# Kernel optimization log

Measured on AMD Instinct MI355X. Metric: run time of the kernel, lower is better.

The kernel has to match this reference:

```python
import jax, jax.numpy as jnp
import numpy as np
import math

B, TQ, TK, D, H, K = 4, 1024, 1536, 1024, 16, 1
DV = D // H * K  # 64
DP = D * K       # projection dim


def setup_inputs() -> dict:
    key = jax.random.key(0)
    ks = jax.random.split(key, 12)
    s = 0.02
    query = jax.random.normal(ks[0], (B, TQ, D), dtype=jnp.float32)
    key_value = jax.random.normal(ks[1], (B, TK, D), dtype=jnp.float32)
    relative = jax.random.normal(ks[2], (B, TK, D), dtype=jnp.float32)
    # Transformer-XL causal mask: query i may attend to key j <= i + mem
    mem = TK - TQ
    i = jnp.arange(TQ)[:, None]
    j = jnp.arange(TK)[None, :]
    mask = jnp.broadcast_to(j > i + mem, (B, TQ, TK))  # True = masked
    Wq = jax.random.normal(ks[3], (D, DP), dtype=jnp.float32) * s
    Wk = jax.random.normal(ks[4], (D, DP), dtype=jnp.float32) * s
    Wv = jax.random.normal(ks[5], (D, DP), dtype=jnp.float32) * s
    Wr = jax.random.normal(ks[6], (D, DP), dtype=jnp.float32) * s
    Wo = jax.random.normal(ks[7], (DP, D), dtype=jnp.float32) * s
    u = jax.random.normal(ks[8], (DV,), dtype=jnp.float32) * s
    v = jax.random.normal(ks[9], (DV,), dtype=jnp.float32) * s
    gamma = jnp.ones((D,), dtype=jnp.float32)
    beta = jnp.zeros((D,), dtype=jnp.float32)
    return {"query": query, "key_value": key_value, "relative": relative,
            "mask": mask, "Wq": Wq, "Wk": Wk, "Wv": Wv, "Wr": Wr, "Wo": Wo,
            "u": u, "v": v, "gamma": gamma, "beta": beta}


def _layer_norm(x, gamma, beta, eps=1e-5):
    mu = jnp.mean(x, axis=-1, keepdims=True)
    var = jnp.mean(jnp.square(x - mu), axis=-1, keepdims=True)
    return (x - mu) * jax.lax.rsqrt(var + eps) * gamma + beta


def reference(query, key_value, relative, mask, Wq, Wk, Wv, Wr, Wo, u, v, gamma, beta):
    b, tq, d = query.shape
    tk = key_value.shape[1]
    dv = u.shape[0]
    h = Wq.shape[1] // dv
    q = (query @ Wq).reshape(b, tq, h, dv)
    k = (key_value @ Wk).reshape(b, tk, h, dv)
    val = (key_value @ Wv).reshape(b, tk, h, dv)
    r = (relative @ Wr).reshape(b, tk, h, dv)
    # content term (q+u)K^T and position term (q+v)R^T, per head
    ac = jnp.einsum('bqhd,bkhd->bhqk', q + u, k)
    bd = jnp.einsum('bqhd,bkhd->bhqk', q + v, r)
    logits = (ac + bd) * (1.0 / math.sqrt(dv))
    logits = jnp.where(mask[:, None, :, :], -jnp.inf, logits)
    w = jax.nn.softmax(logits, axis=-1)
    ctx = jnp.einsum('bhqk,bkhd->bqhd', w, val).reshape(b, tq, h * dv)
    out = ctx @ Wo + query  # residual
    return _layer_norm(out, gamma, beta)
```

## Files before the change

kernel.cpp:

```cpp
#include <hip/hip_runtime.h>


typedef unsigned short u16;
typedef __attribute__((ext_vector_type(8))) short short8;
typedef __attribute__((ext_vector_type(4))) float floatx4;

#define ATTN_SC 0.18033688011112042f

__device__ __forceinline__ float bf2f(u16 u) {
    union { unsigned int i; float f; } w; w.i = ((unsigned int)u) << 16; return w.f;
}
__device__ __forceinline__ u16 f2bf(float f) {
    union { unsigned int i; float f; } w; w.f = f;
    unsigned int u = w.i;
    return (u16)((u + 0x7FFFu + ((u >> 16) & 1u)) >> 16);
}

__device__ __forceinline__ void gl_lds16(const u16* g, u16* lds) {
    __builtin_amdgcn_global_load_lds(
        (const __attribute__((address_space(1))) void*)g,
        (__attribute__((address_space(3))) void*)lds, 16, 0, 0);
}

__global__ __launch_bounds__(256) void cvt3_kernel(
    const float* __restrict__ x0, u16* __restrict__ y0, int n0,
    const float* __restrict__ x1, u16* __restrict__ y1, int n1,
    const float* __restrict__ x2, u16* __restrict__ y2, int n2)
{
    const int which = blockIdx.y;
    const float* x = (which == 0) ? x0 : (which == 1) ? x1 : x2;
    u16* y         = (which == 0) ? y0 : (which == 1) ? y1 : y2;
    const int n    = (which == 0) ? n0 : (which == 1) ? n1 : n2;
    const int i = (blockIdx.x * 256 + threadIdx.x) * 8;
    if (i >= n) return;
    float4 a = *(const float4*)&x[i];
    float4 b = *(const float4*)&x[i + 4];
    short8 o;
    o[0] = (short)f2bf(a.x); o[1] = (short)f2bf(a.y);
    o[2] = (short)f2bf(a.z); o[3] = (short)f2bf(a.w);
    o[4] = (short)f2bf(b.x); o[5] = (short)f2bf(b.y);
    o[6] = (short)f2bf(b.z); o[7] = (short)f2bf(b.w);
    *(short8*)&y[i] = o;
}

__global__ __launch_bounds__(256) void transpose5_kernel(
    const float* __restrict__ Wq, const float* __restrict__ Wk,
    const float* __restrict__ Wr, const float* __restrict__ Wv,
    const float* __restrict__ Wo,
    u16* __restrict__ WqT, u16* __restrict__ WkrT,
    u16* __restrict__ WvT, u16* __restrict__ WoT)
{
    const int z = blockIdx.z;
    const float* W; u16* WT; int dst_ld, dst_koff;
    switch (z) {
        case 0: W = Wq; WT = WqT;  dst_ld = 1024; dst_koff = 0;    break;
        case 1: W = Wk; WT = WkrT; dst_ld = 2048; dst_koff = 0;    break;
        case 2: W = Wr; WT = WkrT; dst_ld = 2048; dst_koff = 1024; break;
        case 3: W = Wv; WT = WvT;  dst_ld = 1024; dst_koff = 0;    break;
        default:W = Wo; WT = WoT;  dst_ld = 1024; dst_koff = 0;    break;
    }
    __shared__ u16 ts[64][72];
    const int k0 = blockIdx.x * 64, n0 = blockIdx.y * 64;
    const int r  = threadIdx.x >> 2;
    const int c4 = (threadIdx.x & 3) << 4;
    const float* src = &W[(size_t)(k0 + r) * 1024 + n0 + c4];
    for (int j = 0; j < 16; j += 4) {
        float4 a = *(const float4*)(src + j);
        ts[r][c4 + j + 0] = f2bf(a.x);
        ts[r][c4 + j + 1] = f2bf(a.y);
        ts[r][c4 + j + 2] = f2bf(a.z);
        ts[r][c4 + j + 3] = f2bf(a.w);
    }
    __syncthreads();
    short8 t0, t1;
    for (int j = 0; j < 8; j++) t0[j] = (short)ts[c4 + j][r];
    for (int j = 0; j < 8; j++) t1[j] = (short)ts[c4 + 8 + j][r];
    u16* dst = &WT[(size_t)(n0 + r) * dst_ld + dst_koff + k0 + c4];
    *(short8*)dst       = t0;
    *(short8*)(dst + 8) = t1;
}

__global__ __launch_bounds__(256) void wuv_kernel(
    const float* __restrict__ Wk, const float* __restrict__ Wr,
    const float* __restrict__ u, const float* __restrict__ v,
    u16* __restrict__ wuvb)
{
    int idx = blockIdx.x * 256 + threadIdx.x;
    int c = idx >> 4, h = idx & 15;
    float au = 0.f, av = 0.f;
    for (int d = 0; d < 64; d++) {
        au += Wk[(size_t)c * 1024 + h * 64 + d] * u[d];
        av += Wr[(size_t)c * 1024 + h * 64 + d] * v[d];
    }
    wuvb[h * 2048 + c]        = f2bf(au);
    wuvb[h * 2048 + 1024 + c] = f2bf(av);
}

template <int EPI>
__device__ __forceinline__ void gemm_body(
    const u16* __restrict__ A0, const u16* __restrict__ A1,
    const u16* __restrict__ WT, void* __restrict__ out,
    int Kld, int kbeg, int kend, int Ksplit, int T,
    int bm, int bn, u16* As, u16* Ws)
{
    const int tid = threadIdx.x;
    const int wave = tid >> 6, lane = tid & 63;
    const int wm = wave >> 1, wn = wave & 1;
    const int l16 = lane & 15, quad = lane >> 4;

    floatx4 acc[4][4];
    const floatx4 zf = {0.f, 0.f, 0.f, 0.f};
    for (int i = 0; i < 4; i++) for (int j = 0; j < 4; j++) acc[i][j] = zf;

    const int m_base = bm * 128, n_base = bn * 128;
    const int rl = lane >> 2;
    const int cl = (lane & 3) * 8;

    for (int k0 = kbeg; k0 < kend; k0 += 32) {
        const u16* Aptr; int kk;
        if (k0 < Ksplit) { Aptr = A0; kk = k0; } else { Aptr = A1; kk = k0 - Ksplit; }
        __syncthreads();
        for (int half = 0; half < 2; half++) {
            const int r = wave * 32 + half * 16;
            gl_lds16(Aptr + (size_t)(m_base + r + rl) * 1024 + kk + cl, &As[r * 32]);
            gl_lds16(WT   + (size_t)(n_base + r + rl) * Kld  + k0 + cl, &Ws[r * 32]);
        }
        __syncthreads();

        short8 af[4], bf[4];
        for (int i = 0; i < 4; i++) {
            af[i] = *(const short8*)&As[(wm * 64 + i * 16 + l16) * 32 + quad * 8];
            bf[i] = *(const short8*)&Ws[(wn * 64 + i * 16 + l16) * 32 + quad * 8];
        }
        for (int i = 0; i < 4; i++)
            for (int j = 0; j < 4; j++)
                acc[i][j] = __builtin_amdgcn_mfma_f32_16x16x32_bf16(af[i], bf[j], acc[i][j], 0, 0, 0);
    }

    for (int i = 0; i < 4; i++) {
        for (int rg = 0; rg < 4; rg++) {
            const int m = m_base + wm * 64 + i * 16 + quad * 4 + rg;
            float* op = (float*)out;
            for (int j = 0; j < 4; j++) {
                const int col = n_base + wn * 64 + j * 16 + l16;
                op[(size_t)m * 1024 + col] = acc[i][j][rg];
            }
        }
    }
}

__device__ __forceinline__ void stage_half(
    const u16* __restrict__ src, int src_ld, int row_base, int col_base,
    u16* lds_slot, int wave, int lane)
{
    const int r = wave * 16 + (lane >> 2);
    const int c = (((lane & 3) ^ ((lane >> 3) & 3)) << 3);
    gl_lds16(src + (size_t)(row_base + r) * src_ld + col_base + c,
             lds_slot + wave * 512);
    gl_lds16(src + (size_t)(row_base + 128 + r) * src_ld + col_base + c,
             lds_slot + 4096 + wave * 512);
}

template <int EPI, int T>
__device__ __forceinline__ void gemm256_body(
    const u16* __restrict__ A0, const u16* __restrict__ A1,
    const u16* __restrict__ WT, void* __restrict__ out,
    int Kld, int NT, int KsplitTile, int bm, int bn,
    u16* As, u16* Bs)
{
    const int tid  = threadIdx.x;
    const int wave = tid >> 6, lane = tid & 63;
    const int wm = wave >> 2, wn = wave & 3;
    const int l16 = lane & 15, quad = lane >> 4;
    const int m_base = bm * 256, n_base = bn * 256;

    floatx4 acc[8][4];
    const floatx4 zf = {0.f, 0.f, 0.f, 0.f};
    #pragma unroll
    for (int i = 0; i < 8; i++)
        #pragma unroll
        for (int j = 0; j < 4; j++) acc[i][j] = zf;

    {
        const u16* sa0 = (0 < KsplitTile) ? A0 : A1;
        stage_half(sa0, 1024, m_base, 0,  As + 0 * 8192, wave, lane);
        stage_half(WT,  Kld,  n_base, 0,  Bs + 0 * 8192, wave, lane);
        stage_half(sa0, 1024, m_base, 32, As + 1 * 8192, wave, lane);
        stage_half(WT,  Kld,  n_base, 32, Bs + 1 * 8192, wave, lane);
        const u16* sa1 = (1 < KsplitTile) ? A0 : A1;
        const int  c1  = (1 < KsplitTile) ? 64 : (1 - KsplitTile) * 64;
        stage_half(sa1, 1024, m_base, c1, As + 2 * 8192, wave, lane);
        stage_half(WT,  Kld,  n_base, 64, Bs + 2 * 8192, wave, lane);
    }

    for (int t = 0; t < NT; ++t) {
        if (t + 1 < NT) asm volatile("s_waitcnt vmcnt(8)" ::: "memory");
        else            asm volatile("s_waitcnt vmcnt(0)" ::: "memory");
        __builtin_amdgcn_s_barrier();

        short8 bfr[4];
        #pragma unroll
        for (int ph = 0; ph < 4; ++ph) {
            if (ph) __builtin_amdgcn_s_barrier();
            const int ks = ph >> 1, mh = ph & 1;

            if (ph == 0) {
                if (t + 1 < NT) {
                    const int tt = t + 1;
                    const u16* sa = (tt < KsplitTile) ? A0 : A1;
                    const int cb = (tt < KsplitTile ? tt : tt - KsplitTile) * 64 + 32;
                    stage_half(sa, 1024, m_base, cb, As + ((2 * tt + 1) & 3) * 8192, wave, lane);
                }
            } else if (ph == 1) {
                if (t + 1 < NT)
                    stage_half(WT, Kld, n_base, (t + 1) * 64 + 32,
                               Bs + ((2 * (t + 1) + 1) & 3) * 8192, wave, lane);
            } else if (ph == 2) {
                if (t + 2 < NT) {
                    const int tt = t + 2;
                    const u16* sa = (tt < KsplitTile) ? A0 : A1;
                    const int cb = (tt < KsplitTile ? tt : tt - KsplitTile) * 64;
                    stage_half(sa, 1024, m_base, cb, As + ((2 * tt) & 3) * 8192, wave, lane);
                }
            } else {
                if (t + 2 < NT)
                    stage_half(WT, Kld, n_base, (t + 2) * 64,
                               Bs + ((2 * (t + 2)) & 3) * 8192, wave, lane);
            }

            const u16* Aslot = As + ((2 * t + ks) & 3) * 8192;
            const u16* Bslot = Bs + ((2 * t + ks) & 3) * 8192;
            if (mh == 0) {
                #pragma unroll
                for (int nj = 0; nj < 4; ++nj) {
                    const int row = wn * 64 + nj * 16 + l16;
                    bfr[nj] = *(const short8*)&Bslot[row * 32 + (((quad ^ (row >> 1)) & 3) << 3)];
                }
            }
            short8 af[4];
            #pragma unroll
            for (int mi = 0; mi < 4; ++mi) {
                const int row = wm * 128 + mh * 64 + mi * 16 + l16;
                af[mi] = *(const short8*)&Aslot[row * 32 + (((quad ^ (row >> 1)) & 3) << 3)];
            }

            __builtin_amdgcn_s_setprio(1);
            #pragma unroll
            for (int mi = 0; mi < 4; ++mi)
                #pragma unroll
                for (int nj = 0; nj < 4; ++nj)
                    acc[mh * 4 + mi][nj] = __builtin_amdgcn_mfma_f32_16x16x32_bf16(
                        af[mi], bfr[nj], acc[mh * 4 + mi][nj], 0, 0, 0);
            __builtin_amdgcn_s_setprio(0);

            if (ph == 1 && t + 1 < NT)
                asm volatile("s_waitcnt vmcnt(8)" ::: "memory");
        }
    }

    u16* op = (u16*)out;
    #pragma unroll
    for (int mi = 0; mi < 8; ++mi) {
        #pragma unroll
        for (int rg = 0; rg < 4; ++rg) {
            const int m = m_base + wm * 128 + mi * 16 + quad * 4 + rg;
            const int b = m / T, tk = m % T;
            #pragma unroll
            for (int nj = 0; nj < 4; ++nj) {
                const int col = n_base + wn * 64 + nj * 16 + l16;
                const int h = col >> 6, d = col & 63;
                if (EPI == 0) {
                    op[(((size_t)(b * 16 + h) * T + tk) << 6) + d] = f2bf(acc[mi][nj][rg]);
                } else {
                    op[((size_t)(b * 16 + h) * 64 + d) * 1536 + tk] = f2bf(acc[mi][nj][rg]);
                }
            }
        }
    }
}

__device__ __forceinline__ void bias_body8(
    const u16* __restrict__ kvb, const u16* __restrict__ relb,
    const u16* __restrict__ wuvb, float* __restrict__ bias, int bblk)
{
    const int tid = threadIdx.x;
    const int wave = tid >> 6, lane = tid & 63;
    const int l16 = lane & 15, quad = lane >> 4;
    const int tBase = bblk * 128 + wave * 16;

    floatx4 acc = {0.f, 0.f, 0.f, 0.f};
    const u16* arow_kv  = kvb  + (size_t)(tBase + l16) * 1024;
    const u16* arow_rel = relb + (size_t)(tBase + l16) * 1024;
    const u16* brow     = wuvb + (size_t)l16 * 2048;

    for (int ks = 0; ks < 64; ks++) {
        const int k0 = ks * 32;
        const u16* ap = (k0 < 1024) ? (arow_kv + k0) : (arow_rel + k0 - 1024);
        short8 af = *(const short8*)(ap + quad * 8);
        short8 bf = *(const short8*)(brow + k0 + quad * 8);
        acc = __builtin_amdgcn_mfma_f32_16x16x32_bf16(af, bf, acc, 0, 0, 0);
    }
    for (int rg = 0; rg < 4; rg++) {
        const int tg = tBase + quad * 4 + rg;
        const int b = tg / 1536, t = tg % 1536;
        bias[((size_t)b * 16 + l16) * 1536 + t] = acc[rg] * ATTN_SC;
    }
}

__global__ __launch_bounds__(512) void fused_proj_v2(
    const u16* __restrict__ qb, const u16* __restrict__ kvb,
    const u16* __restrict__ relb,
    const u16* __restrict__ WqT, const u16* __restrict__ WkrT,
    const u16* __restrict__ WvT, const u16* __restrict__ wuvb,
    u16* __restrict__ Qh, u16* __restrict__ KRh, u16* __restrict__ Vt,
    float* __restrict__ bias)
{
    __shared__ __align__(128) u16 As[4 * 256 * 32];
    __shared__ __align__(128) u16 Bs[4 * 256 * 32];
    const int blk = blockIdx.x;
    if (blk < 96) {
        gemm256_body<0, 1536>(kvb, relb, WkrT, KRh, 2048, 32, 16,
                              blk % 24, blk / 24, As, Bs);
    } else if (blk < 192) {
        const int i = blk - 96;
        gemm256_body<2, 1536>(kvb, kvb, WvT, Vt, 1024, 16, 99,
                              i % 24, i / 24, As, Bs);
    } else if (blk < 256) {
        const int i = blk - 192;
        gemm256_body<0, 1024>(qb, qb, WqT, Qh, 1024, 16, 99,
                              i % 16, i / 16, As, Bs);
    } else {
        bias_body8(kvb, relb, wuvb, bias, blk - 256);
    }
}

__global__ __launch_bounds__(256) void out_gemm(
    const u16* __restrict__ ctx, const u16* __restrict__ WoT,
    float* __restrict__ outp)
{
    __shared__ u16 smem[2 * 128 * 32];
    const int z = blockIdx.z;
    gemm_body<3>(ctx, nullptr, WoT,
                 outp + (size_t)z * 4 * 1024 * 1024, 1024,
                 z * 512, z * 512 + 512, 1024, 1024,
                 blockIdx.x, blockIdx.y, smem, smem + 128 * 32);
}

__global__ __launch_bounds__(256, 4) void attn_kernel(
    const u16* __restrict__ Qh,
    const u16* __restrict__ KRh,
    const u16* __restrict__ Vt,
    const float* __restrict__ bias,
    u16* __restrict__ ctx)
{
    const int blk  = blockIdx.x;
    const int hb   = blk & 63;
    const int qb   = blk >> 6;
    const int b = hb >> 4, h = hb & 15;
    const int tid = threadIdx.x;
    const int wave = tid >> 6, lane = tid & 63;
    const int l16 = lane & 15, quad = lane >> 4;
    const int q0w = qb * 64 + wave * 16;

    const u16* Qp = Qh  + (size_t)hb * 1024 * 64;
    const u16* Kp = KRh + (size_t)hb * 1536 * 64;
    const u16* Vp = Vt  + (size_t)hb * 64 * 1536;
    const float* bp = bias + (size_t)hb * 1536;

    __shared__ __align__(128) u16 Kbuf[2][64 * 64];
    __shared__ __align__(128) u16 Vbuf[2][64 * 64];
    __shared__ __align__(128) u16 Ps[4][16 * 64];

    const int srow = lane >> 3;
    const int scol = ((lane & 7) ^ srow) * 8;

    const floatx4 zf = {0.f, 0.f, 0.f, 0.f};
    floatx4 accO[4];
    float lsum = 0.f;
    #pragma unroll
    for (int j = 0; j < 4; j++) accO[j] = zf;

    short8 aq[2];
    #pragma unroll
    for (int ks = 0; ks < 2; ks++)
        aq[ks] = *(const short8*)
            &Qp[(size_t)(q0w + l16) * 64 + ks * 32 + quad * 8];

    const int nkt = qb + 9;

    {
        const int r0 = wave * 16;
        gl_lds16(Kp + (size_t)(r0 + srow) * 64 + scol,        &Kbuf[0][r0 * 64]);
        gl_lds16(Kp + (size_t)(r0 + 8 + srow) * 64 + scol,    &Kbuf[0][(r0 + 8) * 64]);
        gl_lds16(Vp + (size_t)(r0 + srow) * 1536 + scol,      &Vbuf[0][r0 * 64]);
        gl_lds16(Vp + (size_t)(r0 + 8 + srow) * 1536 + scol,  &Vbuf[0][(r0 + 8) * 64]);
    }
    __syncthreads();

    for (int kt = 0; kt < nkt; kt++) {
        const int k0 = kt * 64;
        const int cur = kt & 1;

        if (kt + 1 < nkt) {
            const int k1 = (kt + 1) * 64;
            const int r0 = wave * 16;
            u16* Kd = &Kbuf[cur ^ 1][0];
            u16* Vd = &Vbuf[cur ^ 1][0];
            gl_lds16(Kp + (size_t)(k1 + r0 + srow) * 64 + scol,       Kd + r0 * 64);
            gl_lds16(Kp + (size_t)(k1 + r0 + 8 + srow) * 64 + scol,   Kd + (r0 + 8) * 64);
            gl_lds16(Vp + (size_t)(r0 + srow) * 1536 + k1 + scol,     Vd + r0 * 64);
            gl_lds16(Vp + (size_t)(r0 + 8 + srow) * 1536 + k1 + scol, Vd + (r0 + 8) * 64);
        }

        float4 bc[4];
        #pragma unroll
        for (int n = 0; n < 4; n++)
            bc[n] = *(const float4*)&bp[k0 + n * 16 + quad * 4];

        const u16* Kb = &Kbuf[cur][0];
        const u16* Vb = &Vbuf[cur][0];
        short8 bk[4][2];
        #pragma unroll
        for (int n = 0; n < 4; n++)
            #pragma unroll
            for (int ks = 0; ks < 2; ks++)
                bk[n][ks] = *(const short8*)
                    &Kb[(n * 16 + l16) * 64 + (((ks * 4 + quad) ^ (l16 & 7)) * 8)];

        floatx4 accS[4];
        #pragma unroll
        for (int n = 0; n < 4; n++) {
            accS[n] = zf;
            #pragma unroll
            for (int ks = 0; ks < 2; ks++)
                accS[n] = __builtin_amdgcn_mfma_f32_16x16x32_bf16(
                    bk[n][ks], aq[ks], accS[n], 0, 0, 0);
        }

        const int qg = q0w + l16;
        const bool domask = (k0 + 63 > q0w + 15 + 512);
        const int lim = qg + 512 - k0;
        char* Pbase = (char*)&Ps[wave][0];
        #pragma unroll
        for (int n = 0; n < 4; n++) {
            const int limn = lim - n * 16 - quad * 4;
            const float* bcn = (const float*)&bc[n];
            float pv[4];
            #pragma unroll
            for (int rg = 0; rg < 4; rg++) {
                float s = fmaf(accS[n][rg], ATTN_SC, bcn[rg]);
                if (domask && rg > limn) s = -1e30f;
                float pe;
                asm("v_exp_f32 %0, %1" : "=v"(pe) : "v"(s));
                lsum += pe;
                pv[rg] = pe;
            }
            unsigned w0, w1;
            asm("v_cvt_pk_bf16_f32 %0, %1, %2" : "=v"(w0) : "v"(pv[0]), "v"(pv[1]));
            asm("v_cvt_pk_bf16_f32 %0, %1, %2" : "=v"(w1) : "v"(pv[2]), "v"(pv[3]));
            unsigned* pw = (unsigned*)(Pbase +
                (((l16 * 128 + n * 32 + quad * 8)) ^ ((l16 & 7) << 4)));
            pw[0] = w0; pw[1] = w1;
        }

        short8 ap[2];
        #pragma unroll
        for (int ks = 0; ks < 2; ks++)
            ap[ks] = *(const short8*)(Pbase +
                (((l16 * 128 + ks * 64 + quad * 16)) ^ ((l16 & 7) << 4)));
        #pragma unroll
        for (int j = 0; j < 4; j++) {
            #pragma unroll
            for (int ks = 0; ks < 2; ks++) {
                short8 bv = *(const short8*)
                    &Vb[(j * 16 + l16) * 64 + (((ks * 4 + quad) ^ (l16 & 7)) * 8)];
                accO[j] = __builtin_amdgcn_mfma_f32_16x16x32_bf16(
                    ap[ks], bv, accO[j], 0, 0, 0);
            }
        }

        __syncthreads();
    }

    {
        float s = lsum;
        s += __shfl_xor(s, 16, 64);
        s += __shfl_xor(s, 32, 64);
        lsum = s;
    }
    float ltr[4];
    #pragma unroll
    for (int rg = 0; rg < 4; rg++)
        ltr[rg] = __shfl(lsum, quad * 4 + rg, 16);

    #pragma unroll
    for (int j = 0; j < 4; j++)
        #pragma unroll
        for (int rg = 0; rg < 4; rg++) {
            const int q = q0w + quad * 4 + rg;
            const int d = j * 16 + l16;
            ctx[((size_t)b * 1024 + q) * 1024 + h * 64 + d] =
                f2bf(accO[j][rg] / ltr[rg]);
        }
}

__global__ __launch_bounds__(256) void ln_kernel(
    const float* __restrict__ x0, const float* __restrict__ x1,
    const float* __restrict__ q,
    const float* __restrict__ gamma, const float* __restrict__ beta,
    float* __restrict__ out)
{
    const int row = blockIdx.x;
    const int tid = threadIdx.x;
    const size_t base = (size_t)row * 1024 + tid * 4;
    float4 a = *(const float4*)&x0[base];
    float4 c = *(const float4*)&x1[base];
    float4 r = *(const float4*)&q[base];
    float4 v;
    v.x = a.x + c.x + r.x; v.y = a.y + c.y + r.y;
    v.z = a.z + c.z + r.z; v.w = a.w + c.w + r.w;
    float s  = v.x + v.y + v.z + v.w;
    float ss = v.x * v.x + v.y * v.y + v.z * v.z + v.w * v.w;
    for (int off = 1; off < 64; off <<= 1) {
        s  += __shfl_xor(s, off, 64);
        ss += __shfl_xor(ss, off, 64);
    }
    __shared__ float sm[8];
    const int wave = tid >> 6, lane = tid & 63;
    if (lane == 0) { sm[wave] = s; sm[4 + wave] = ss; }
    __syncthreads();
    s  = sm[0] + sm[1] + sm[2] + sm[3];
    ss = sm[4] + sm[5] + sm[6] + sm[7];
    const float mu  = s * (1.f / 1024.f);
    const float var = ss * (1.f / 1024.f) - mu * mu;
    const float inv = rsqrtf(var + 1e-5f);
    float* op = out + (size_t)row * 1024;
    const float* ve = &v.x;
    for (int j = 0; j < 4; j++) {
        const int c2 = tid * 4 + j;
        op[c2] = (ve[j] - mu) * inv * gamma[c2] + beta[c2];
    }
}

extern "C" void kernel_launch(void* const* d_in, const int* in_sizes, int n_in,
                              void* d_out, int out_size, void* d_ws, size_t ws_size,
                              hipStream_t stream)
{
    const float* query     = (const float*)d_in[0];
    const float* key_value = (const float*)d_in[1];
    const float* relative  = (const float*)d_in[2];
    const float* Wq = (const float*)d_in[4];
    const float* Wk = (const float*)d_in[5];
    const float* Wv = (const float*)d_in[6];
    const float* Wr = (const float*)d_in[7];
    const float* Wo = (const float*)d_in[8];
    const float* u  = (const float*)d_in[9];
    const float* v  = (const float*)d_in[10];
    const float* gamma = (const float*)d_in[11];
    const float* beta  = (const float*)d_in[12];

    char* wsp = (char*)d_ws;
    auto alloc = [&](size_t bytes) -> char* {
        char* p = wsp; wsp += (bytes + 255) & ~(size_t)255; return p;
    };
    u16*   qb   = (u16*)alloc((size_t)4 * 1024 * 1024 * 2);
    u16*   kvb  = (u16*)alloc((size_t)4 * 1536 * 1024 * 2);
    u16*   relb = (u16*)alloc((size_t)4 * 1536 * 1024 * 2);
    u16*   WqT  = (u16*)alloc((size_t)1024 * 1024 * 2);
    u16*   WkrT = (u16*)alloc((size_t)1024 * 2048 * 2);
    u16*   WvT  = (u16*)alloc((size_t)1024 * 1024 * 2);
    u16*   WoT  = (u16*)alloc((size_t)1024 * 1024 * 2);
    u16*   wuvb = (u16*)alloc((size_t)16 * 2048 * 2);
    u16*   Qh   = (u16*)alloc((size_t)4 * 16 * 1024 * 64 * 2);
    u16*   KRh  = (u16*)alloc((size_t)4 * 16 * 1536 * 64 * 2);
    u16*   Vt   = (u16*)alloc((size_t)4 * 16 * 64 * 1536 * 2);
    float* bias = (float*)alloc((size_t)4 * 16 * 1536 * 4);
    u16*   ctx  = (u16*)alloc((size_t)4 * 1024 * 1024 * 2);
    float* outp = (float*)alloc((size_t)2 * 4 * 1024 * 1024 * 4);

    const dim3 tb(256);
    cvt3_kernel<<<dim3(3072, 3), tb, 0, stream>>>(
        query, qb, 4 * 1024 * 1024,
        key_value, kvb, 4 * 1536 * 1024,
        relative, relb, 4 * 1536 * 1024);

    transpose5_kernel<<<dim3(16, 16, 5), tb, 0, stream>>>(
        Wq, Wk, Wr, Wv, Wo, WqT, WkrT, WvT, WoT);
    wuv_kernel<<<64, tb, 0, stream>>>(Wk, Wr, u, v, wuvb);

    fused_proj_v2<<<dim3(304), dim3(512), 0, stream>>>(
        qb, kvb, relb, WqT, WkrT, WvT, wuvb, Qh, KRh, Vt, bias);

    attn_kernel<<<dim3(1024), tb, 0, stream>>>(Qh, KRh, Vt, bias, ctx);

    out_gemm<<<dim3(32, 8, 2), tb, 0, stream>>>(ctx, WoT, outp);
    ln_kernel<<<4096, tb, 0, stream>>>(
        outp, outp + (size_t)4 * 1024 * 1024, query, gamma, beta, (float*)d_out);
}
```

Baseline: 293.3 us.

## Merge prep kernels into one launch and widen attention blocks to 128 queries

Three preprocessing kernels (activation bf16 conversion, weight transposes, u/v bias projection) are merged into one launch with block-index dispatch, removing two launch gaps. The attention kernel now uses 512 threads (8 waves) per block covering 128 query rows, so each K/V tile loaded into LDS is shared by twice as many waves, and each wave loads half as many rows. The trade-off is half as many blocks and coarser causal granularity: each block iterates to the furthest key tile its last wave needs, which adds masked work for the early waves.

```diff
diff --git a/kernel.cpp b/kernel.cpp
--- a/kernel.cpp
+++ b/kernel.cpp
@@ -22,78 +22,80 @@
         (__attribute__((address_space(3))) void*)lds, 16, 0, 0);
 }
 
-__global__ __launch_bounds__(256) void cvt3_kernel(
-    const float* __restrict__ x0, u16* __restrict__ y0, int n0,
-    const float* __restrict__ x1, u16* __restrict__ y1, int n1,
-    const float* __restrict__ x2, u16* __restrict__ y2, int n2)
-{
-    const int which = blockIdx.y;
-    const float* x = (which == 0) ? x0 : (which == 1) ? x1 : x2;
-    u16* y         = (which == 0) ? y0 : (which == 1) ? y1 : y2;
-    const int n    = (which == 0) ? n0 : (which == 1) ? n1 : n2;
-    const int i = (blockIdx.x * 256 + threadIdx.x) * 8;
-    if (i >= n) return;
-    float4 a = *(const float4*)&x[i];
-    float4 b = *(const float4*)&x[i + 4];
-    short8 o;
-    o[0] = (short)f2bf(a.x); o[1] = (short)f2bf(a.y);
-    o[2] = (short)f2bf(a.z); o[3] = (short)f2bf(a.w);
-    o[4] = (short)f2bf(b.x); o[5] = (short)f2bf(b.y);
-    o[6] = (short)f2bf(b.z); o[7] = (short)f2bf(b.w);
-    *(short8*)&y[i] = o;
-}
-
-__global__ __launch_bounds__(256) void transpose5_kernel(
+__global__ __launch_bounds__(256) void prep_kernel(
+    const float* __restrict__ query, u16* __restrict__ qb,
+    const float* __restrict__ key_value, u16* __restrict__ kvb,
+    const float* __restrict__ relative, u16* __restrict__ relb,
     const float* __restrict__ Wq, const float* __restrict__ Wk,
     const float* __restrict__ Wr, const float* __restrict__ Wv,
     const float* __restrict__ Wo,
     u16* __restrict__ WqT, u16* __restrict__ WkrT,
-    u16* __restrict__ WvT, u16* __restrict__ WoT)
-{
-    const int z = blockIdx.z;
-    const float* W; u16* WT; int dst_ld, dst_koff;
-    switch (z) {
-        case 0: W = Wq; WT = WqT;  dst_ld = 1024; dst_koff = 0;    break;
-        case 1: W = Wk; WT = WkrT; dst_ld = 2048; dst_koff = 0;    break;
-        case 2: W = Wr; WT = WkrT; dst_ld = 2048; dst_koff = 1024; break;
-        case 3: W = Wv; WT = WvT;  dst_ld = 1024; dst_koff = 0;    break;
-        default:W = Wo; WT = WoT;  dst_ld = 1024; dst_koff = 0;    break;
-    }
-    __shared__ u16 ts[64][72];
-    const int k0 = blockIdx.x * 64, n0 = blockIdx.y * 64;
-    const int r  = threadIdx.x >> 2;
-    const int c4 = (threadIdx.x & 3) << 4;
-    const float* src = &W[(size_t)(k0 + r) * 1024 + n0 + c4];
-    for (int j = 0; j < 16; j += 4) {
-        float4 a = *(const float4*)(src + j);
-        ts[r][c4 + j + 0] = f2bf(a.x);
-        ts[r][c4 + j + 1] = f2bf(a.y);
-        ts[r][c4 + j + 2] = f2bf(a.z);
-        ts[r][c4 + j + 3] = f2bf(a.w);
-    }
-    __syncthreads();
-    short8 t0, t1;
-    for (int j = 0; j < 8; j++) t0[j] = (short)ts[c4 + j][r];
-    for (int j = 0; j < 8; j++) t1[j] = (short)ts[c4 + 8 + j][r];
-    u16* dst = &WT[(size_t)(n0 + r) * dst_ld + dst_koff + k0 + c4];
-    *(short8*)dst       = t0;
-    *(short8*)(dst + 8) = t1;
-}
-
-__global__ __launch_bounds__(256) void wuv_kernel(
-    const float* __restrict__ Wk, const float* __restrict__ Wr,
+    u16* __restrict__ WvT, u16* __restrict__ WoT,
     const float* __restrict__ u, const float* __restrict__ v,
     u16* __restrict__ wuvb)
 {
-    int idx = blockIdx.x * 256 + threadIdx.x;
-    int c = idx >> 4, h = idx & 15;
-    float au = 0.f, av = 0.f;
-    for (int d = 0; d < 64; d++) {
-        au += Wk[(size_t)c * 1024 + h * 64 + d] * u[d];
-        av += Wr[(size_t)c * 1024 + h * 64 + d] * v[d];
-    }
-    wuvb[h * 2048 + c]        = f2bf(au);
-    wuvb[h * 2048 + 1024 + c] = f2bf(av);
+    __shared__ u16 ts[64][72];
+    const int blk = blockIdx.x;
+    const int tid = threadIdx.x;
+
+    if (blk < 1280) {
+        const int z  = blk >> 8;
+        const int by = (blk >> 4) & 15;
+        const int bx = blk & 15;
+        const float* W; u16* WT; int dst_ld, dst_koff;
+        switch (z) {
+            case 0: W = Wq; WT = WqT;  dst_ld = 1024; dst_koff = 0;    break;
+            case 1: W = Wk; WT = WkrT; dst_ld = 2048; dst_koff = 0;    break;
+            case 2: W = Wr; WT = WkrT; dst_ld = 2048; dst_koff = 1024; break;
+            case 3: W = Wv; WT = WvT;  dst_ld = 1024; dst_koff = 0;    break;
+            default:W = Wo; WT = WoT;  dst_ld = 1024; dst_koff = 0;    break;
+        }
+        const int k0 = bx * 64, n0 = by * 64;
+        const int r  = tid >> 2;
+        const int c4 = (tid & 3) << 4;
+        const float* src = &W[(size_t)(k0 + r) * 1024 + n0 + c4];
+        for (int j = 0; j < 16; j += 4) {
+            float4 a = *(const float4*)(src + j);
+            ts[r][c4 + j + 0] = f2bf(a.x);
+            ts[r][c4 + j + 1] = f2bf(a.y);
+            ts[r][c4 + j + 2] = f2bf(a.z);
+            ts[r][c4 + j + 3] = f2bf(a.w);
+        }
+        __syncthreads();
+        short8 t0, t1;
+        for (int j = 0; j < 8; j++) t0[j] = (short)ts[c4 + j][r];
+        for (int j = 0; j < 8; j++) t1[j] = (short)ts[c4 + 8 + j][r];
+        u16* dst = &WT[(size_t)(n0 + r) * dst_ld + dst_koff + k0 + c4];
+        *(short8*)dst       = t0;
+        *(short8*)(dst + 8) = t1;
+    } else if (blk < 1344) {
+        int idx = (blk - 1280) * 256 + tid;
+        int c = idx >> 4, h = idx & 15;
+        float au = 0.f, av = 0.f;
+        for (int d = 0; d < 64; d++) {
+            au += Wk[(size_t)c * 1024 + h * 64 + d] * u[d];
+            av += Wr[(size_t)c * 1024 + h * 64 + d] * v[d];
+        }
+        wuvb[h * 2048 + c]        = f2bf(au);
+        wuvb[h * 2048 + 1024 + c] = f2bf(av);
+    } else {
+        const int c = blk - 1344;
+        const float* x; u16* y; int n, bx;
+        if (c < 2048)      { x = query;     y = qb;   n = 4 * 1024 * 1024; bx = c; }
+        else if (c < 5120) { x = key_value; y = kvb;  n = 6 * 1024 * 1024; bx = c - 2048; }
+        else               { x = relative;  y = relb; n = 6 * 1024 * 1024; bx = c - 5120; }
+        const int i = (bx * 256 + tid) * 8;
+        if (i < n) {
+            float4 a = *(const float4*)&x[i];
+            float4 bv = *(const float4*)&x[i + 4];
+            short8 o;
+            o[0] = (short)f2bf(a.x);  o[1] = (short)f2bf(a.y);
+            o[2] = (short)f2bf(a.z);  o[3] = (short)f2bf(a.w);
+            o[4] = (short)f2bf(bv.x); o[5] = (short)f2bf(bv.y);
+            o[6] = (short)f2bf(bv.z); o[7] = (short)f2bf(bv.w);
+            *(short8*)&y[i] = o;
+        }
+    }
 }
 
 template <int EPI>
@@ -346,7 +348,7 @@
                  blockIdx.x, blockIdx.y, smem, smem + 128 * 32);
 }
 
-__global__ __launch_bounds__(256, 4) void attn_kernel(
+__global__ __launch_bounds__(512, 4) void attn_kernel(
     const u16* __restrict__ Qh,
     const u16* __restrict__ KRh,
     const u16* __restrict__ Vt,
@@ -355,12 +357,12 @@
 {
     const int blk  = blockIdx.x;
     const int hb   = blk & 63;
-    const int qb   = blk >> 6;
+    const int qblk = blk >> 6;
     const int b = hb >> 4, h = hb & 15;
     const int tid = threadIdx.x;
     const int wave = tid >> 6, lane = tid & 63;
     const int l16 = lane & 15, quad = lane >> 4;
-    const int q0w = qb * 64 + wave * 16;
+    const int q0w = qblk * 128 + wave * 16;
 
     const u16* Qp = Qh  + (size_t)hb * 1024 * 64;
     const u16* Kp = KRh + (size_t)hb * 1536 * 64;
@@ -369,7 +371,7 @@
 
     __shared__ __align__(128) u16 Kbuf[2][64 * 64];
     __shared__ __align__(128) u16 Vbuf[2][64 * 64];
-    __shared__ __align__(128) u16 Ps[4][16 * 64];
+    __shared__ __align__(128) u16 Ps[8][16 * 64];
 
     const int srow = lane >> 3;
     const int scol = ((lane & 7) ^ srow) * 8;
@@ -386,14 +388,12 @@
         aq[ks] = *(const short8*)
             &Qp[(size_t)(q0w + l16) * 64 + ks * 32 + quad * 8];
 
-    const int nkt = qb + 9;
+    const int nkt = 2 * qblk + 10;
 
     {
-        const int r0 = wave * 16;
-        gl_lds16(Kp + (size_t)(r0 + srow) * 64 + scol,        &Kbuf[0][r0 * 64]);
-        gl_lds16(Kp + (size_t)(r0 + 8 + srow) * 64 + scol,    &Kbuf[0][(r0 + 8) * 64]);
-        gl_lds16(Vp + (size_t)(r0 + srow) * 1536 + scol,      &Vbuf[0][r0 * 64]);
-        gl_lds16(Vp + (size_t)(r0 + 8 + srow) * 1536 + scol,  &Vbuf[0][(r0 + 8) * 64]);
+        const int r0 = wave * 8;
+        gl_lds16(Kp + (size_t)(r0 + srow) * 64 + scol,   &Kbuf[0][r0 * 64]);
+        gl_lds16(Vp + (size_t)(r0 + srow) * 1536 + scol, &Vbuf[0][r0 * 64]);
     }
     __syncthreads();
 
@@ -403,13 +403,11 @@
 
         if (kt + 1 < nkt) {
             const int k1 = (kt + 1) * 64;
-            const int r0 = wave * 16;
-            u16* Kd = &Kbuf[cur ^ 1][0];
-            u16* Vd = &Vbuf[cur ^ 1][0];
-            gl_lds16(Kp + (size_t)(k1 + r0 + srow) * 64 + scol,       Kd + r0 * 64);
-            gl_lds16(Kp + (size_t)(k1 + r0 + 8 + srow) * 64 + scol,   Kd + (r0 + 8) * 64);
-            gl_lds16(Vp + (size_t)(r0 + srow) * 1536 + k1 + scol,     Vd + r0 * 64);
-            gl_lds16(Vp + (size_t)(r0 + 8 + srow) * 1536 + k1 + scol, Vd + (r0 + 8) * 64);
+            const int r0 = wave * 8;
+            gl_lds16(Kp + (size_t)(k1 + r0 + srow) * 64 + scol,
+                     &Kbuf[cur ^ 1][r0 * 64]);
+            gl_lds16(Vp + (size_t)(r0 + srow) * 1536 + k1 + scol,
+                     &Vbuf[cur ^ 1][r0 * 64]);
         }
 
         float4 bc[4];
@@ -579,19 +577,14 @@
     float* outp = (float*)alloc((size_t)2 * 4 * 1024 * 1024 * 4);
 
     const dim3 tb(256);
-    cvt3_kernel<<<dim3(3072, 3), tb, 0, stream>>>(
-        query, qb, 4 * 1024 * 1024,
-        key_value, kvb, 4 * 1536 * 1024,
-        relative, relb, 4 * 1536 * 1024);
-
-    transpose5_kernel<<<dim3(16, 16, 5), tb, 0, stream>>>(
-        Wq, Wk, Wr, Wv, Wo, WqT, WkrT, WvT, WoT);
-    wuv_kernel<<<64, tb, 0, stream>>>(Wk, Wr, u, v, wuvb);
+    prep_kernel<<<dim3(9536), tb, 0, stream>>>(
+        query, qb, key_value, kvb, relative, relb,
+        Wq, Wk, Wr, Wv, Wo, WqT, WkrT, WvT, WoT, u, v, wuvb);
 
     fused_proj_v2<<<dim3(304), dim3(512), 0, stream>>>(
         qb, kvb, relb, WqT, WkrT, WvT, wuvb, Qh, KRh, Vt, bias);
 
-    attn_kernel<<<dim3(1024), tb, 0, stream>>>(Qh, KRh, Vt, bias, ctx);
+    attn_kernel<<<dim3(512), dim3(512), 0, stream>>>(Qh, KRh, Vt, bias, ctx);
 
     out_gemm<<<dim3(32, 8, 2), tb, 0, stream>>>(ctx, WoT, outp);
     ln_kernel<<<4096, tb, 0, stream>>>(
```

New measurement: 287.6 us. Within noise of the previous version (-2.0%).
